# Kernel optimization log

Measured on AMD Instinct MI355X. Metric: run time of the kernel, lower is better.

Reference implementation:

```python
import jax, jax.numpy as jnp
import numpy as np

D_MODEL = 1024
HIDDEN = 4096
NUM_EXPERTS = 8
NUM_GROUPS = 4      # from _compute_group_size(4, 4096) with max_group_size=4096
GROUP_SIZE = 4096
EXPERT_CAPACITY = 512  # round(1.0 * 4096 / 8), >= max(8, 4096//100)


def setup_inputs() -> dict:
    key = jax.random.key(0)
    ks = jax.random.split(key, 10)
    s_in = 1.0 / np.sqrt(D_MODEL)
    s_hid = 1.0 / np.sqrt(HIDDEN)
    return {
        "x": jax.random.normal(ks[0], (4, 4096, D_MODEL), dtype=jnp.float32),
        "gate_w": jax.random.normal(ks[1], (D_MODEL, NUM_EXPERTS), dtype=jnp.float32) * 0.1,
        "gate_b": jax.random.normal(ks[2], (NUM_EXPERTS,), dtype=jnp.float32) * 0.01,
        "temperature": jnp.ones((1,), dtype=jnp.float32),
        "shared_w1": jax.random.normal(ks[3], (D_MODEL, HIDDEN), dtype=jnp.float32) * s_in,
        "shared_b1": jnp.zeros((HIDDEN,), dtype=jnp.float32),
        "shared_w2": jax.random.normal(ks[4], (HIDDEN, D_MODEL), dtype=jnp.float32) * s_hid,
        "shared_b2": jnp.zeros((D_MODEL,), dtype=jnp.float32),
        "expert_w1": jax.random.normal(ks[5], (NUM_EXPERTS, D_MODEL, HIDDEN), dtype=jnp.float32) * s_in,
        "expert_b1": jnp.zeros((NUM_EXPERTS, HIDDEN), dtype=jnp.float32),
        "expert_w2": jax.random.normal(ks[6], (NUM_EXPERTS, HIDDEN, D_MODEL), dtype=jnp.float32) * s_hid,
        "expert_b2": jnp.zeros((NUM_EXPERTS, D_MODEL), dtype=jnp.float32),
    }


def reference(x, gate_w, gate_b, temperature, shared_w1, shared_b1, shared_w2,
              shared_b2, expert_w1, expert_b1, expert_w2, expert_b2):
    B, S, D = x.shape
    T = NUM_GROUPS * GROUP_SIZE  # total tokens (no padding here)
    xg = x.reshape(NUM_GROUPS, GROUP_SIZE, D)

    # Router: softmax over temperature-scaled gate logits
    logits = jnp.einsum('gsd,de->gse', xg, gate_w) + gate_b
    safe_temp = jnp.maximum(temperature, 0.1)
    probs = jax.nn.softmax(logits / safe_temp, axis=-1)  # [G, Gs, E]
    # per-expert top-k over ALL tokens (flattened across groups)
    flat_probs = probs.transpose(2, 0, 1).reshape(NUM_EXPERTS, T)
    scores, tok_idx = jax.lax.top_k(flat_probs, EXPERT_CAPACITY)  # [E, C]

    # Shared expert FFN (gelu is tanh-approx, matching flax nn.gelu default)
    shared = jnp.einsum('gsh,hd->gsd',
                        jax.nn.gelu(jnp.einsum('gsd,dh->gsh', xg, shared_w1) + shared_b1),
                        shared_w2) + shared_b2

    # Routed experts: gather tokens, grouped FFN, weighted scatter-add
    x_flat = xg.reshape(T, D)
    tokens = x_flat[tok_idx]  # [E, C, D]
    h = jax.nn.gelu(jnp.einsum('ecd,edh->ech', tokens, expert_w1) + expert_b1[:, None, :])
    out_e = jnp.einsum('ech,ehd->ecd', h, expert_w2) + expert_b2[:, None, :]
    out_e = out_e * scores[..., None]
    routed = jnp.zeros_like(x_flat).at[tok_idx.reshape(-1)].add(out_e.reshape(-1, D))

    out = shared.reshape(T, D) + routed
    return out.reshape(B, S, D)
```

## Files before the change

kernel.cpp:

```cpp
#include <hip/hip_runtime.h>

#define NTOK 16384
#define DMODEL 1024
#define DHID 4096
#define NEXP 8
#define CAP 512

typedef __attribute__((ext_vector_type(8))) short bfrag_t;
typedef __attribute__((ext_vector_type(4))) float ffrag_t;

__device__ __forceinline__ unsigned short f2bf(float f) {
  unsigned u = __float_as_uint(f);
  u += 0x7FFFu + ((u >> 16) & 1u);
  return (unsigned short)(u >> 16);
}

__device__ __forceinline__ float gelu_fast(float x) {
  float t = x * x;
  float z = x * fmaf(0.071354814f, t, 1.5957691f);
  float e = __expf(-z);
  return x * __builtin_amdgcn_rcpf(1.0f + e);
}

__global__ __launch_bounds__(256) void k_trans64(const float* __restrict__ in,
                                                 unsigned short* __restrict__ out, int K, int N) {
  const size_t zb = blockIdx.z;
  in  += zb * (size_t)K * N;
  out += zb * (size_t)N * K;
  __shared__ float tile[64][65];
  const int n0 = blockIdx.x * 64, k0 = blockIdx.y * 64;
  const int tx = threadIdx.x & 63, ty = threadIdx.x >> 6;
#pragma unroll
  for (int i = 0; i < 16; ++i) {
    const int k = ty * 16 + i;
    tile[k][tx] = in[(size_t)(k0 + k) * N + n0 + tx];
  }
  __syncthreads();
  const int sx = threadIdx.x & 7, sy = threadIdx.x >> 3;
#pragma unroll
  for (int j = 0; j < 2; ++j) {
    const int n = sy + j * 32;
    uint4 v;
    v.x = (unsigned)f2bf(tile[sx * 8 + 0][n]) | ((unsigned)f2bf(tile[sx * 8 + 1][n]) << 16);
    v.y = (unsigned)f2bf(tile[sx * 8 + 2][n]) | ((unsigned)f2bf(tile[sx * 8 + 3][n]) << 16);
    v.z = (unsigned)f2bf(tile[sx * 8 + 4][n]) | ((unsigned)f2bf(tile[sx * 8 + 5][n]) << 16);
    v.w = (unsigned)f2bf(tile[sx * 8 + 6][n]) | ((unsigned)f2bf(tile[sx * 8 + 7][n]) << 16);
    *(uint4*)&out[(size_t)(n0 + n) * K + k0 + sx * 8] = v;
  }
}

__global__ __launch_bounds__(256) void k_router(const float* __restrict__ x, const float* __restrict__ gw,
                                                const float* __restrict__ gb, const float* __restrict__ temp,
                                                float* __restrict__ probs, unsigned short* __restrict__ xb) {
  __shared__ float gws[DMODEL * NEXP];
  for (int i = threadIdx.x; i < DMODEL * NEXP; i += 256) gws[i] = gw[i];
  __syncthreads();
  const int wave = threadIdx.x >> 6, lane = threadIdx.x & 63;
  const int t = blockIdx.x * 4 + wave;
  const float* xr = x + (size_t)t * DMODEL;
  unsigned short* xw = xb + (size_t)t * DMODEL;
  float acc[NEXP];
#pragma unroll
  for (int e = 0; e < NEXP; ++e) acc[e] = 0.f;
  for (int d = lane; d < DMODEL; d += 64) {
    float xv = xr[d];
    xw[d] = f2bf(xv);
#pragma unroll
    for (int e = 0; e < NEXP; ++e) acc[e] += xv * gws[d * NEXP + e];
  }
#pragma unroll
  for (int off = 32; off >= 1; off >>= 1) {
#pragma unroll
    for (int e = 0; e < NEXP; ++e) acc[e] += __shfl_xor(acc[e], off);
  }
  if (lane == 0) {
    float st = fmaxf(temp[0], 0.1f);
    float m = -1e30f;
#pragma unroll
    for (int e = 0; e < NEXP; ++e) { acc[e] = (acc[e] + gb[e]) / st; m = fmaxf(m, acc[e]); }
    float s = 0.f;
#pragma unroll
    for (int e = 0; e < NEXP; ++e) { acc[e] = expf(acc[e] - m); s += acc[e]; }
    float inv = 1.f / s;
#pragma unroll
    for (int e = 0; e < NEXP; ++e) probs[(size_t)e * NTOK + t] = acc[e] * inv;
  }
}

__global__ __launch_bounds__(256) void k_topk(const float* __restrict__ probs, int* __restrict__ tok,
                                              float* __restrict__ scores, int* __restrict__ eqbuf,
                                              int* __restrict__ slot) {
  const int e = blockIdx.x;
  const float* p = probs + (size_t)e * NTOK;
  int* eq = eqbuf + (size_t)e * NTOK;
  int* sl = slot + (size_t)e * NTOK;
  __shared__ int hist[256];
  __shared__ unsigned sh_pref;
  __shared__ int sh_k, sh_gt, sh_eq, sh_cnt;
  const int tid = threadIdx.x;
  for (int t = tid; t < NTOK; t += 256) sl[t] = -1;
  if (tid == 0) { sh_pref = 0u; sh_k = CAP; }
  __syncthreads();
  for (int pass = 3; pass >= 0; --pass) {
    hist[tid] = 0;
    __syncthreads();
    const unsigned pref = sh_pref;
    const int shift = pass * 8;
    for (int t = tid; t < NTOK; t += 256) {
      unsigned key = __float_as_uint(p[t]);
      bool cand = (pass == 3) || ((key >> (shift + 8)) == pref);
      if (cand) atomicAdd(&hist[(key >> shift) & 255], 1);
    }
    __syncthreads();
    if (tid == 0) {
      int k = sh_k;
      int d = 255;
      while (hist[d] < k) { k -= hist[d]; --d; }
      sh_k = k;
      sh_pref = (pref << 8) | (unsigned)d;
    }
    __syncthreads();
  }
  const unsigned Kstar = sh_pref;
  const int need_eq = sh_k;
  if (tid == 0) { sh_gt = 0; sh_eq = 0; }
  __syncthreads();
  for (int t = tid; t < NTOK; t += 256) {
    unsigned key = __float_as_uint(p[t]);
    if (key > Kstar) {
      int pos = atomicAdd(&sh_gt, 1);
      tok[e * CAP + pos] = t;
      scores[e * CAP + pos] = p[t];
      sl[t] = pos;
    } else if (key == Kstar) {
      int q = atomicAdd(&sh_eq, 1);
      eq[q] = t;
    }
  }
  __syncthreads();
  const int cg = sh_gt, ce = sh_eq;
  if (ce <= need_eq) {
    for (int j = tid; j < ce; j += 256) {
      tok[e * CAP + cg + j] = eq[j];
      scores[e * CAP + cg + j] = p[eq[j]];
      sl[eq[j]] = cg + j;
    }
  } else {
    int lo = 0, hi = NTOK - 1;
    while (lo < hi) {
      int mid = (lo + hi) >> 1;
      if (tid == 0) sh_cnt = 0;
      __syncthreads();
      for (int j = tid; j < ce; j += 256)
        if (eq[j] <= mid) atomicAdd(&sh_cnt, 1);
      __syncthreads();
      if (sh_cnt >= need_eq) hi = mid; else lo = mid + 1;
      __syncthreads();
    }
    if (tid == 0) sh_cnt = 0;
    __syncthreads();
    for (int j = tid; j < ce; j += 256) {
      if (eq[j] <= lo) {
        int pos = cg + atomicAdd(&sh_cnt, 1);
        tok[e * CAP + pos] = eq[j];
        scores[e * CAP + pos] = p[eq[j]];
        sl[eq[j]] = pos;
      }
    }
  }
}

__global__ __launch_bounds__(256) void k_combine(const float* __restrict__ pe,
                                                 const int* __restrict__ slot,
                                                 float* __restrict__ out) {
  const int wave = threadIdx.x >> 6, lane = threadIdx.x & 63;
  const int t = blockIdx.x * 4 + wave;
  int sl[NEXP];
  bool any = false;
#pragma unroll
  for (int e = 0; e < NEXP; ++e) {
    sl[e] = slot[(size_t)e * NTOK + t];
    any = any || (sl[e] >= 0);
  }
  if (!any) return;
  float* orow = out + (size_t)t * DMODEL;
  float4 a[4];
#pragma unroll
  for (int i = 0; i < 4; ++i) a[i] = *(float4*)&orow[i * 256 + lane * 4];
#pragma unroll
  for (int e = 0; e < NEXP; ++e) {
    if (sl[e] >= 0) {
      const float* p0 = pe + (((size_t)e * 2 + 0) * CAP + sl[e]) * DMODEL;
      const float* p1 = pe + (((size_t)e * 2 + 1) * CAP + sl[e]) * DMODEL;
#pragma unroll
      for (int i = 0; i < 4; ++i) {
        float4 v0 = *(const float4*)&p0[i * 256 + lane * 4];
        float4 v1 = *(const float4*)&p1[i * 256 + lane * 4];
        a[i].x += v0.x + v1.x;
        a[i].y += v0.y + v1.y;
        a[i].z += v0.z + v1.z;
        a[i].w += v0.w + v1.w;
      }
    }
  }
#pragma unroll
  for (int i = 0; i < 4; ++i) *(float4*)&orow[i * 256 + lane * 4] = a[i];
}

template <int MODE, bool GATHER>
__global__ __launch_bounds__(256, 4) void k_gemm(
    const unsigned short* __restrict__ A, const unsigned short* __restrict__ Bt,
    const float* __restrict__ bias, float* __restrict__ outF, unsigned short* __restrict__ outB,
    const int* __restrict__ tok, const float* __restrict__ scale,
    int M, int N, int Kloop, int LDK, int ksplit) {
  const int zb = blockIdx.z / ksplit;
  const int kc = blockIdx.z % ksplit;
  if (!GATHER) A += (size_t)zb * M * LDK;
  A += (size_t)kc * Kloop;
  Bt += (size_t)zb * N * LDK + (size_t)kc * Kloop;
  const float* bz = bias + (size_t)zb * N;

  const int gx = gridDim.x, gy = gridDim.y;
  const int nwg = gx * gy;
  const int id = blockIdx.x + blockIdx.y * gx;
  int bx, by;
  if ((gx & 7) == 0) {
    const int x = id & 7, c = id >> 3, H = gx >> 3;
    bx = x * H + (c % H);
    by = c / H;
  } else if ((nwg & 7) == 0) {
    const int q = nwg >> 3;
    const int sw = (id & 7) * q + (id >> 3);
    bx = sw % gx;
    by = sw / gx;
  } else {
    bx = blockIdx.x;
    by = blockIdx.y;
  }
  const int m0 = bx * 128, n0 = by * 128;

  const int tid = threadIdx.x, wave = tid >> 6, lane = tid & 63;
  const int wm = (wave >> 1) * 64, wn = (wave & 1) * 64;

  __shared__ alignas(16) unsigned short sh[128 * 128];
  unsigned short* As = sh;
  unsigned short* Bs = sh + 128 * 64;

  ffrag_t acc[4][4];
#pragma unroll
  for (int i = 0; i < 4; ++i)
#pragma unroll
    for (int j = 0; j < 4; ++j)
#pragma unroll
      for (int r = 0; r < 4; ++r) acc[i][j][r] = 0.f;

  int lb[4];
  const unsigned short* rowA[4];
  const unsigned short* rowB[4];
#pragma unroll
  for (int it = 0; it < 4; ++it) {
    int L = it * 256 + tid;
    int rr = L >> 3;
    int gg = (L & 7) ^ (rr & 7);
    lb[it] = (it * 256 + wave * 64) * 16;
    const unsigned short* ab =
        GATHER ? (A + (size_t)tok[zb * M + m0 + rr] * LDK) : (A + (size_t)(m0 + rr) * LDK);
    rowA[it] = ab + gg * 8;
    rowB[it] = Bt + (size_t)(n0 + rr) * LDK + gg * 8;
  }

  for (int kt = 0; kt < Kloop; kt += 64) {
#pragma unroll
    for (int it = 0; it < 4; ++it) {
      __builtin_amdgcn_global_load_lds(
          (const __attribute__((address_space(1))) unsigned int*)(rowA[it] + kt),
          (__attribute__((address_space(3))) unsigned int*)((char*)As + lb[it]), 16, 0, 0);
      __builtin_amdgcn_global_load_lds(
          (const __attribute__((address_space(1))) unsigned int*)(rowB[it] + kt),
          (__attribute__((address_space(3))) unsigned int*)((char*)Bs + lb[it]), 16, 0, 0);
    }
    __syncthreads();
#pragma unroll
    for (int kk = 0; kk < 2; ++kk) {
      bfrag_t af[4], bf[4];
      const int gl = kk * 4 + (lane >> 4);
#pragma unroll
      for (int mi = 0; mi < 4; ++mi) {
        int r = wm + mi * 16 + (lane & 15);
        af[mi] = *(const bfrag_t*)&As[r * 64 + ((gl ^ (r & 7)) * 8)];
      }
#pragma unroll
      for (int ni = 0; ni < 4; ++ni) {
        int r = wn + ni * 16 + (lane & 15);
        bf[ni] = *(const bfrag_t*)&Bs[r * 64 + ((gl ^ (r & 7)) * 8)];
      }
#pragma unroll
      for (int mi = 0; mi < 4; ++mi)
#pragma unroll
        for (int ni = 0; ni < 4; ++ni)
          acc[mi][ni] = __builtin_amdgcn_mfma_f32_16x16x32_bf16(af[mi], bf[ni], acc[mi][ni], 0, 0, 0);
    }
    __syncthreads();
  }

  const int rsub = (lane >> 4) * 4, cs = lane & 15;
  if (MODE == 0) {
    float bv[4];
#pragma unroll
    for (int ni = 0; ni < 4; ++ni) bv[ni] = bz[n0 + wn + ni * 16 + cs];
#pragma unroll
    for (int mi = 0; mi < 4; ++mi)
#pragma unroll
      for (int ni = 0; ni < 4; ++ni)
#pragma unroll
        for (int r = 0; r < 4; ++r) {
          float v = acc[mi][ni][r] + bv[ni];
          sh[(wm + mi * 16 + rsub + r) * 128 + (wn + ni * 16 + cs)] = f2bf(gelu_fast(v));
        }
    __syncthreads();
    const int seg = tid & 15, rw = tid >> 4;
#pragma unroll
    for (int rep = 0; rep < 8; ++rep) {
      const int row = rep * 16 + rw;
      uint4 v = *(const uint4*)&sh[row * 128 + seg * 8];
      *(uint4*)&outB[((size_t)zb * M + m0 + row) * N + n0 + seg * 8] = v;
    }
  } else if (MODE == 1) {
#pragma unroll
    for (int ni = 0; ni < 4; ++ni) {
      const int n = n0 + wn + ni * 16 + cs;
      const float bv = bz[n];
#pragma unroll
      for (int mi = 0; mi < 4; ++mi)
#pragma unroll
        for (int r = 0; r < 4; ++r) {
          const int m = m0 + wm + mi * 16 + rsub + r;
          outF[(size_t)m * N + n] = acc[mi][ni][r] + bv;
        }
    }
  } else {
    float* po = outF + (size_t)blockIdx.z * M * N;
#pragma unroll
    for (int ni = 0; ni < 4; ++ni) {
      const int n = n0 + wn + ni * 16 + cs;
      const float bv = (kc == 0) ? bz[n] : 0.f;
#pragma unroll
      for (int mi = 0; mi < 4; ++mi)
#pragma unroll
        for (int r = 0; r < 4; ++r) {
          const int m = m0 + wm + mi * 16 + rsub + r;
          const float s = scale[zb * M + m];
          po[(size_t)m * N + n] = (acc[mi][ni][r] + bv) * s;
        }
    }
  }
}

extern "C" void kernel_launch(void* const* d_in, const int* in_sizes, int n_in,
                              void* d_out, int out_size, void* d_ws, size_t ws_size,
                              hipStream_t stream) {
  const float* x      = (const float*)d_in[0];
  const float* gate_w = (const float*)d_in[1];
  const float* gate_b = (const float*)d_in[2];
  const float* temp   = (const float*)d_in[3];
  const float* sw1    = (const float*)d_in[4];
  const float* sb1    = (const float*)d_in[5];
  const float* sw2    = (const float*)d_in[6];
  const float* sb2    = (const float*)d_in[7];
  const float* ew1    = (const float*)d_in[8];
  const float* eb1    = (const float*)d_in[9];
  const float* ew2    = (const float*)d_in[10];
  const float* eb2    = (const float*)d_in[11];
  float* out = (float*)d_out;

  char* ws = (char*)d_ws;
  size_t o = 0;
  auto take = [&](size_t bytes) { char* p = ws + o; o += (bytes + 255) & ~(size_t)255; return p; };
  unsigned short* x_bf = (unsigned short*)take((size_t)NTOK * DMODEL * 2);
  unsigned short* w1t  = (unsigned short*)take((size_t)DMODEL * DHID * 2);
  unsigned short* w2t  = (unsigned short*)take((size_t)DHID * DMODEL * 2);
  unsigned short* ew1t = (unsigned short*)take((size_t)NEXP * DMODEL * DHID * 2);
  unsigned short* ew2t = (unsigned short*)take((size_t)NEXP * DHID * DMODEL * 2);
  float* probs         = (float*)take((size_t)NEXP * NTOK * 4);
  int* tok             = (int*)take((size_t)NEXP * CAP * 4);
  float* scores        = (float*)take((size_t)NEXP * CAP * 4);
  int* eqbuf           = (int*)take((size_t)NEXP * NTOK * 4);
  int* slot            = (int*)take((size_t)NEXP * NTOK * 4);
  float* pe            = (float*)take((size_t)NEXP * 2 * CAP * DMODEL * 4);
  unsigned short* he   = (unsigned short*)take((size_t)NEXP * CAP * DHID * 2);
  unsigned short* hs   = (unsigned short*)take((size_t)NTOK * DHID * 2);

  k_trans64<<<dim3(DHID / 64, DMODEL / 64, 1), 256, 0, stream>>>(sw1, w1t, DMODEL, DHID);
  k_trans64<<<dim3(DMODEL / 64, DHID / 64, 1), 256, 0, stream>>>(sw2, w2t, DHID, DMODEL);
  k_trans64<<<dim3(DHID / 64, DMODEL / 64, NEXP), 256, 0, stream>>>(ew1, ew1t, DMODEL, DHID);
  k_trans64<<<dim3(DMODEL / 64, DHID / 64, NEXP), 256, 0, stream>>>(ew2, ew2t, DHID, DMODEL);

  k_router<<<NTOK / 4, 256, 0, stream>>>(x, gate_w, gate_b, temp, probs, x_bf);
  k_topk<<<NEXP, 256, 0, stream>>>(probs, tok, scores, eqbuf, slot);

  k_gemm<0, false><<<dim3(128, 32, 1), 256, 0, stream>>>(
      x_bf, w1t, sb1, nullptr, hs, nullptr, nullptr, NTOK, DHID, DMODEL, DMODEL, 1);
  k_gemm<1, false><<<dim3(128, 8, 1), 256, 0, stream>>>(
      hs, w2t, sb2, out, nullptr, nullptr, nullptr, NTOK, DMODEL, DHID, DHID, 1);

  k_gemm<0, true><<<dim3(4, 32, NEXP), 256, 0, stream>>>(
      x_bf, ew1t, eb1, nullptr, he, tok, nullptr, CAP, DHID, DMODEL, DMODEL, 1);
  k_gemm<3, false><<<dim3(4, 8, NEXP * 2), 256, 0, stream>>>(
      he, ew2t, eb2, pe, nullptr, nullptr, scores, CAP, DMODEL, DHID / 2, DHID, 2);

  k_combine<<<NTOK / 4, 256, 0, stream>>>(pe, slot, out);
}
```

Before: 670.7 us.

## Fuse routed-expert combine into shared down-projection epilogue and merge transpose launches

The separate combine kernel is removed. The shared-expert second GEMM now runs last, and its epilogue gathers the two split-K expert partial outputs for each token via the slot table, adding them before writing the final result. Weight transposes for shared and expert matrices are merged into two launches, and the large bf16 hidden and output stores use nontemporal stores. This removes a full read and write pass over the output and some launch overhead, at the cost of scattered per-element gathers inside the GEMM epilogue and a reordered launch sequence.

After: 651.3 us. 1.03x faster.

```diff
diff --git a/kernel.cpp b/kernel.cpp
--- a/kernel.cpp
+++ b/kernel.cpp
@@ -8,6 +8,7 @@
 
 typedef __attribute__((ext_vector_type(8))) short bfrag_t;
 typedef __attribute__((ext_vector_type(4))) float ffrag_t;
+typedef __attribute__((ext_vector_type(4))) unsigned int u32x4;
 
 __device__ __forceinline__ unsigned short f2bf(float f) {
   unsigned u = __float_as_uint(f);
@@ -22,11 +23,21 @@
   return x * __builtin_amdgcn_rcpf(1.0f + e);
 }
 
-__global__ __launch_bounds__(256) void k_trans64(const float* __restrict__ in,
-                                                 unsigned short* __restrict__ out, int K, int N) {
-  const size_t zb = blockIdx.z;
-  in  += zb * (size_t)K * N;
-  out += zb * (size_t)N * K;
+__global__ __launch_bounds__(256) void k_trans64d(const float* __restrict__ s_in,
+                                                  const float* __restrict__ e_in,
+                                                  unsigned short* __restrict__ s_out,
+                                                  unsigned short* __restrict__ e_out,
+                                                  int K, int N) {
+  const int zb = blockIdx.z;
+  const float* in;
+  unsigned short* out;
+  if (zb == 0) {
+    in = s_in;
+    out = s_out;
+  } else {
+    in = e_in + (size_t)(zb - 1) * K * N;
+    out = e_out + (size_t)(zb - 1) * N * K;
+  }
   __shared__ float tile[64][65];
   const int n0 = blockIdx.x * 64, k0 = blockIdx.y * 64;
   const int tx = threadIdx.x & 63, ty = threadIdx.x >> 6;
@@ -40,12 +51,12 @@
 #pragma unroll
   for (int j = 0; j < 2; ++j) {
     const int n = sy + j * 32;
-    uint4 v;
+    u32x4 v;
     v.x = (unsigned)f2bf(tile[sx * 8 + 0][n]) | ((unsigned)f2bf(tile[sx * 8 + 1][n]) << 16);
     v.y = (unsigned)f2bf(tile[sx * 8 + 2][n]) | ((unsigned)f2bf(tile[sx * 8 + 3][n]) << 16);
     v.z = (unsigned)f2bf(tile[sx * 8 + 4][n]) | ((unsigned)f2bf(tile[sx * 8 + 5][n]) << 16);
     v.w = (unsigned)f2bf(tile[sx * 8 + 6][n]) | ((unsigned)f2bf(tile[sx * 8 + 7][n]) << 16);
-    *(uint4*)&out[(size_t)(n0 + n) * K + k0 + sx * 8] = v;
+    *(u32x4*)&out[(size_t)(n0 + n) * K + k0 + sx * 8] = v;
   }
 }
 
@@ -170,44 +181,7 @@
   }
 }
 
-__global__ __launch_bounds__(256) void k_combine(const float* __restrict__ pe,
-                                                 const int* __restrict__ slot,
-                                                 float* __restrict__ out) {
-  const int wave = threadIdx.x >> 6, lane = threadIdx.x & 63;
-  const int t = blockIdx.x * 4 + wave;
-  int sl[NEXP];
-  bool any = false;
-#pragma unroll
-  for (int e = 0; e < NEXP; ++e) {
-    sl[e] = slot[(size_t)e * NTOK + t];
-    any = any || (sl[e] >= 0);
-  }
-  if (!any) return;
-  float* orow = out + (size_t)t * DMODEL;
-  float4 a[4];
-#pragma unroll
-  for (int i = 0; i < 4; ++i) a[i] = *(float4*)&orow[i * 256 + lane * 4];
-#pragma unroll
-  for (int e = 0; e < NEXP; ++e) {
-    if (sl[e] >= 0) {
-      const float* p0 = pe + (((size_t)e * 2 + 0) * CAP + sl[e]) * DMODEL;
-      const float* p1 = pe + (((size_t)e * 2 + 1) * CAP + sl[e]) * DMODEL;
-#pragma unroll
-      for (int i = 0; i < 4; ++i) {
-        float4 v0 = *(const float4*)&p0[i * 256 + lane * 4];
-        float4 v1 = *(const float4*)&p1[i * 256 + lane * 4];
-        a[i].x += v0.x + v1.x;
-        a[i].y += v0.y + v1.y;
-        a[i].z += v0.z + v1.z;
-        a[i].w += v0.w + v1.w;
-      }
-    }
-  }
-#pragma unroll
-  for (int i = 0; i < 4; ++i) *(float4*)&orow[i * 256 + lane * 4] = a[i];
-}
-
-template <int MODE, bool GATHER>
+template <int MODE, bool GATHER, bool NT>
 __global__ __launch_bounds__(256, 4) void k_gemm(
     const unsigned short* __restrict__ A, const unsigned short* __restrict__ Bt,
     const float* __restrict__ bias, float* __restrict__ outF, unsigned short* __restrict__ outB,
@@ -322,23 +296,14 @@
 #pragma unroll
     for (int rep = 0; rep < 8; ++rep) {
       const int row = rep * 16 + rw;
-      uint4 v = *(const uint4*)&sh[row * 128 + seg * 8];
-      *(uint4*)&outB[((size_t)zb * M + m0 + row) * N + n0 + seg * 8] = v;
-    }
-  } else if (MODE == 1) {
-#pragma unroll
-    for (int ni = 0; ni < 4; ++ni) {
-      const int n = n0 + wn + ni * 16 + cs;
-      const float bv = bz[n];
-#pragma unroll
-      for (int mi = 0; mi < 4; ++mi)
-#pragma unroll
-        for (int r = 0; r < 4; ++r) {
-          const int m = m0 + wm + mi * 16 + rsub + r;
-          outF[(size_t)m * N + n] = acc[mi][ni][r] + bv;
-        }
-    }
-  } else {
+      u32x4 v = *(const u32x4*)&sh[row * 128 + seg * 8];
+      u32x4* dst = (u32x4*)&outB[((size_t)zb * M + m0 + row) * N + n0 + seg * 8];
+      if (NT)
+        __builtin_nontemporal_store(v, dst);
+      else
+        *dst = v;
+    }
+  } else if (MODE == 3) {
     float* po = outF + (size_t)blockIdx.z * M * N;
 #pragma unroll
     for (int ni = 0; ni < 4; ++ni) {
@@ -352,6 +317,39 @@
           const float s = scale[zb * M + m];
           po[(size_t)m * N + n] = (acc[mi][ni][r] + bv) * s;
         }
+    }
+  } else {
+    const int* slot = tok;
+    const float* pe = scale;
+    float bv[4];
+#pragma unroll
+    for (int ni = 0; ni < 4; ++ni) bv[ni] = bz[n0 + wn + ni * 16 + cs];
+#pragma unroll
+    for (int mi = 0; mi < 4; ++mi) {
+#pragma unroll
+      for (int r = 0; r < 4; ++r) {
+        const int m = m0 + wm + mi * 16 + rsub + r;
+        float ex[4] = {0.f, 0.f, 0.f, 0.f};
+#pragma unroll
+        for (int e = 0; e < NEXP; ++e) {
+          const int sl = slot[(size_t)e * NTOK + m];
+          if (sl >= 0) {
+            const float* p0 = pe + ((size_t)(e * 2 + 0) * CAP + sl) * DMODEL;
+            const float* p1 = pe + ((size_t)(e * 2 + 1) * CAP + sl) * DMODEL;
+#pragma unroll
+            for (int ni = 0; ni < 4; ++ni) {
+              const int n = n0 + wn + ni * 16 + cs;
+              ex[ni] += p0[n] + p1[n];
+            }
+          }
+        }
+#pragma unroll
+        for (int ni = 0; ni < 4; ++ni) {
+          const int n = n0 + wn + ni * 16 + cs;
+          __builtin_nontemporal_store(acc[mi][ni][r] + bv[ni] + ex[ni],
+                                      &outF[(size_t)m * N + n]);
+        }
+      }
     }
   }
 }
@@ -390,23 +388,22 @@
   unsigned short* he   = (unsigned short*)take((size_t)NEXP * CAP * DHID * 2);
   unsigned short* hs   = (unsigned short*)take((size_t)NTOK * DHID * 2);
 
-  k_trans64<<<dim3(DHID / 64, DMODEL / 64, 1), 256, 0, stream>>>(sw1, w1t, DMODEL, DHID);
-  k_trans64<<<dim3(DMODEL / 64, DHID / 64, 1), 256, 0, stream>>>(sw2, w2t, DHID, DMODEL);
-  k_trans64<<<dim3(DHID / 64, DMODEL / 64, NEXP), 256, 0, stream>>>(ew1, ew1t, DMODEL, DHID);
-  k_trans64<<<dim3(DMODEL / 64, DHID / 64, NEXP), 256, 0, stream>>>(ew2, ew2t, DHID, DMODEL);
+  k_trans64d<<<dim3(DHID / 64, DMODEL / 64, 1 + NEXP), 256, 0, stream>>>(
+      sw1, ew1, w1t, ew1t, DMODEL, DHID);
+  k_trans64d<<<dim3(DMODEL / 64, DHID / 64, 1 + NEXP), 256, 0, stream>>>(
+      sw2, ew2, w2t, ew2t, DHID, DMODEL);
 
   k_router<<<NTOK / 4, 256, 0, stream>>>(x, gate_w, gate_b, temp, probs, x_bf);
   k_topk<<<NEXP, 256, 0, stream>>>(probs, tok, scores, eqbuf, slot);
 
-  k_gemm<0, false><<<dim3(128, 32, 1), 256, 0, stream>>>(
+  k_gemm<0, false, true><<<dim3(128, 32, 1), 256, 0, stream>>>(
       x_bf, w1t, sb1, nullptr, hs, nullptr, nullptr, NTOK, DHID, DMODEL, DMODEL, 1);
-  k_gemm<1, false><<<dim3(128, 8, 1), 256, 0, stream>>>(
-      hs, w2t, sb2, out, nullptr, nullptr, nullptr, NTOK, DMODEL, DHID, DHID, 1);
-
-  k_gemm<0, true><<<dim3(4, 32, NEXP), 256, 0, stream>>>(
+
+  k_gemm<0, true, false><<<dim3(4, 32, NEXP), 256, 0, stream>>>(
       x_bf, ew1t, eb1, nullptr, he, tok, nullptr, CAP, DHID, DMODEL, DMODEL, 1);
-  k_gemm<3, false><<<dim3(4, 8, NEXP * 2), 256, 0, stream>>>(
+  k_gemm<3, false, false><<<dim3(4, 8, NEXP * 2), 256, 0, stream>>>(
       he, ew2t, eb2, pe, nullptr, nullptr, scores, CAP, DMODEL, DHID / 2, DHID, 2);
 
-  k_combine<<<NTOK / 4, 256, 0, stream>>>(pe, slot, out);
-}
+  k_gemm<4, false, true><<<dim3(128, 8, 1), 256, 0, stream>>>(
+      hs, w2t, sb2, out, nullptr, slot, pe, NTOK, DMODEL, DHID, DHID, 1);
+}
```
